# Kernel tuning notes

Measured on AMD Instinct MI355X. Metric: run time of the kernel, lower is better.

The kernel has to match this reference:

```python
import jax, jax.numpy as jnp
import numpy as np

N_NODES = 50000
N_EDGES = 600000
D_IN = 128
H = D_IN // 2  # 64
N_GRAPHS = 500
DIM_TARGET = 1


def setup_inputs() -> dict:
    key = jax.random.key(0)
    ks = jax.random.split(key, 16)
    x = jax.random.normal(ks[0], (N_NODES, D_IN), dtype=jnp.float32)
    edge_index = jax.random.randint(ks[1], (2, N_EDGES), 0, N_NODES, dtype=jnp.int64)
    batch = jnp.sort(jax.random.randint(ks[2], (N_NODES,), 0, N_GRAPHS, dtype=jnp.int64))
    # SAGEConv params: lin_l (neighbor aggregate, with bias), lin_r (root, no bias)
    s = 1.0 / np.sqrt(D_IN)
    Wl = jax.random.uniform(ks[3], (D_IN, H), jnp.float32, -s, s)
    bl = jnp.zeros((H,), jnp.float32)
    Wr = jax.random.uniform(ks[4], (D_IN, H), jnp.float32, -s, s)
    # MLP: 64->32->16->8->1
    dims = [H, H // 2, H // 4, H // 8, DIM_TARGET]
    params = {}
    for i in range(4):
        si = 1.0 / np.sqrt(dims[i])
        params[f"W{i}"] = jax.random.uniform(ks[5 + 2 * i], (dims[i], dims[i + 1]), jnp.float32, -si, si)
        params[f"b{i}"] = jax.random.uniform(ks[6 + 2 * i], (dims[i + 1],), jnp.float32, -si, si)
    return dict(x=x, edge_index=edge_index, batch=batch, Wl=Wl, bl=bl, Wr=Wr, **params)


def reference(x, edge_index, batch, Wl, bl, Wr, W0, b0, W1, b1, W2, b2, W3, b3):
    n_nodes = x.shape[0]
    src, dst = edge_index[0], edge_index[1]
    # SAGEConv mean aggregation: mean of source-node features at each target node
    agg = jax.ops.segment_sum(x[src], dst, num_segments=n_nodes)          # [N, D]
    cnt = jax.ops.segment_sum(jnp.ones((src.shape[0],), x.dtype), dst, num_segments=n_nodes)
    mean_nbr = agg / jnp.maximum(cnt, 1.0)[:, None]
    x1 = mean_nbr @ Wl + bl + x @ Wr                                      # [N, H]
    # global_mean_pool by graph id
    gsum = jax.ops.segment_sum(x1, batch, num_segments=N_GRAPHS)          # [G, H]
    gcnt = jax.ops.segment_sum(jnp.ones((n_nodes,), x.dtype), batch, num_segments=N_GRAPHS)
    h = gsum / jnp.maximum(gcnt, 1.0)[:, None]
    # MLP (dropout is identity in eval mode)
    h = jax.nn.relu(h @ W0 + b0)
    h = jax.nn.relu(h @ W1 + b1)
    h = jax.nn.relu(h @ W2 + b2)
    return h @ W3 + b3
```

## Files before the change

kernel.cpp:

```cpp
#include <hip/hip_runtime.h>
#include <hip/hip_bf16.h>

#define N_NODES  50000
#define N_EDGES  600000
#define D_IN     128
#define H        64
#define N_GRAPHS 500
#define MAXDEG   48

#define PROJ_BLOCKS 782
#define M_TILES     3125
#define SCAT_CHUNKS 512
#define SCAT_BLOCKS (SCAT_CHUNKS * 8)
#define EPC         1172
#define NPS         (N_NODES / 8)
#define GST_BLOCKS  2
#define PX_BLOCKS   500
#define PREP_GRID   (PROJ_BLOCKS + SCAT_BLOCKS + GST_BLOCKS + PX_BLOCKS)

#define SPLIT    16
#define GBLK     (N_GRAPHS * SPLIT)

#define OF_DEG   0
#define MEMSET_B 200704
#define OF_PNP   200704
#define OF_PX    2248704
#define OF_GCNT  2504704
#define OF_GST   2506752
#define OF_COL   2508800
#define OF_YB    7308800

typedef __attribute__((ext_vector_type(8))) short short8;
typedef __attribute__((ext_vector_type(4))) float float4v;

__device__ __forceinline__ float bflo(unsigned int u) { return __uint_as_float(u << 16); }
__device__ __forceinline__ float bfhi(unsigned int u) { return __uint_as_float(u & 0xffff0000u); }
__device__ __forceinline__ unsigned short f2bf(float f) {
    return __bfloat16_as_ushort(__float2bfloat16(f));
}

__global__ __launch_bounds__(256) void prep_kernel(
        const float* __restrict__ x, const float* __restrict__ Wl,
        unsigned short* __restrict__ yb,
        const int* __restrict__ src, const int* __restrict__ dst,
        int* __restrict__ deg, unsigned short* __restrict__ col,
        const int* __restrict__ batch, int* __restrict__ gstart,
        float* __restrict__ Px, int* __restrict__ gcnt) {
    __shared__ float red[512];
    int bid = blockIdx.x, t = threadIdx.x;
    int wave = t >> 6, lane = t & 63;

    if (bid < PROJ_BLOCKS) {
        int mt = bid * 4 + wave;
        if (mt < M_TILES) {
            int c = lane & 15, q = lane >> 4;
            short8 Bf[4][4];
            #pragma unroll
            for (int t4 = 0; t4 < 4; ++t4)
                #pragma unroll
                for (int s4 = 0; s4 < 4; ++s4) {
                    short8 b;
                    #pragma unroll
                    for (int jj = 0; jj < 8; ++jj)
                        b[jj] = (short)f2bf(Wl[(s4 * 32 + q * 8 + jj) * H + t4 * 16 + c]);
                    Bf[t4][s4] = b;
                }
            float4v acc[4] = {};
            const float* xrow = x + ((size_t)mt * 16 + c) * D_IN + q * 8;
            #pragma unroll
            for (int s4 = 0; s4 < 4; ++s4) {
                const float4* ap = (const float4*)(xrow + s4 * 32);
                float4 a0 = ap[0], a1 = ap[1];
                short8 Af;
                Af[0] = (short)f2bf(a0.x); Af[1] = (short)f2bf(a0.y);
                Af[2] = (short)f2bf(a0.z); Af[3] = (short)f2bf(a0.w);
                Af[4] = (short)f2bf(a1.x); Af[5] = (short)f2bf(a1.y);
                Af[6] = (short)f2bf(a1.z); Af[7] = (short)f2bf(a1.w);
                #pragma unroll
                for (int t4 = 0; t4 < 4; ++t4)
                    acc[t4] = __builtin_amdgcn_mfma_f32_16x16x32_bf16(Af, Bf[t4][s4], acc[t4], 0, 0, 0);
            }
            #pragma unroll
            for (int t4 = 0; t4 < 4; ++t4)
                #pragma unroll
                for (int r = 0; r < 4; ++r) {
                    int node = mt * 16 + q * 4 + r;
                    yb[(size_t)node * H + t4 * 16 + c] = f2bf(acc[t4][r]);
                }
        }
    } else if (bid < PROJ_BLOCKS + SCAT_BLOCKS) {
        int shard = bid & 7;
        int chunk = (bid - PROJ_BLOCKS) >> 3;
        int lo = shard * NPS, hi = lo + NPS;
        int e0 = chunk * EPC;
        int e1 = e0 + EPC; if (e1 > N_EDGES) e1 = N_EDGES;
        for (int e = e0 + t; e < e1; e += 256) {
            int d = dst[e];
            if (d >= lo && d < hi) {
                int pos = atomicAdd(&deg[d], 1);
                if (pos < MAXDEG)
                    col[(size_t)d * MAXDEG + pos] = (unsigned short)src[e];
            }
        }
    } else if (bid < PROJ_BLOCKS + SCAT_BLOCKS + GST_BLOCKS) {
        int g = (bid - PROJ_BLOCKS - SCAT_BLOCKS) * 256 + t;
        if (g <= N_GRAPHS) {
            int lo = 0, hi = N_NODES;
            while (lo < hi) {
                int m = (lo + hi) >> 1;
                if (batch[m] < g) lo = m + 1; else hi = m;
            }
            gstart[g] = lo;
        }
    } else {
        int p = bid - PROJ_BLOCKS - SCAT_BLOCKS - GST_BLOCKS;
        int lo = 0, hi = N_NODES;
        while (lo < hi) { int m = (lo + hi) >> 1; if (batch[m] < p) lo = m + 1; else hi = m; }
        int a = lo;
        hi = N_NODES;
        while (lo < hi) { int m = (lo + hi) >> 1; if (batch[m] < p + 1) lo = m + 1; else hi = m; }
        int b = lo;
        float fx = 0.f, fy = 0.f;
        for (int n = a + wave; n < b; n += 4) {
            float2 u = ((const float2*)(x + (size_t)n * D_IN))[lane];
            fx += u.x; fy += u.y;
        }
        red[wave * D_IN + 2 * lane]     = fx;
        red[wave * D_IN + 2 * lane + 1] = fy;
        __syncthreads();
        if (t < D_IN) {
            float v = red[t] + red[D_IN + t] + red[2 * D_IN + t] + red[3 * D_IN + t];
            Px[(size_t)p * D_IN + t] = v;
        }
        if (t == 0) gcnt[p] = b - a;
    }
}

__global__ __launch_bounds__(256) void gather_kernel(
        const unsigned short* __restrict__ yb, const unsigned short* __restrict__ col,
        const int* __restrict__ deg, const int* __restrict__ gstart,
        float* __restrict__ PnP) {
    __shared__ float red[4 * H];
    int bid  = blockIdx.x;
    int wave = threadIdx.x >> 6;
    int lane = threadIdx.x & 63;
    int half = lane >> 5, fp = lane & 31;
    int g = bid >> 4, s = bid & 15;
    int n0 = gstart[g], n1 = gstart[g + 1];
    const unsigned short* yl = yb + 2 * fp;

    float2 pn = make_float2(0.f, 0.f);
    for (int n = n0 + s * 4 + wave; n < n1; n += 4 * SPLIT) {
        int d = deg[n];
        int dl = (d < MAXDEG) ? d : MAXDEG;
        int cidx = (lane < dl) ? (int)col[(size_t)n * MAXDEG + lane] : 0;

        float tx = 0.f, ty = 0.f;
        int j = 0;
        for (; j + 8 <= dl; j += 8) {
            int s0 = __shfl(cidx, j + half),     s1 = __shfl(cidx, j + 2 + half);
            int s2 = __shfl(cidx, j + 4 + half), s3 = __shfl(cidx, j + 6 + half);
            unsigned int u0 = *(const unsigned int*)(yl + (size_t)s0 * H);
            unsigned int u1 = *(const unsigned int*)(yl + (size_t)s1 * H);
            unsigned int u2 = *(const unsigned int*)(yl + (size_t)s2 * H);
            unsigned int u3 = *(const unsigned int*)(yl + (size_t)s3 * H);
            tx += bflo(u0) + bflo(u1) + bflo(u2) + bflo(u3);
            ty += bfhi(u0) + bfhi(u1) + bfhi(u2) + bfhi(u3);
        }
        for (; j + 2 <= dl; j += 2) {
            int s0 = __shfl(cidx, j + half);
            unsigned int u = *(const unsigned int*)(yl + (size_t)s0 * H);
            tx += bflo(u); ty += bfhi(u);
        }
        if (j < dl) {
            int s0 = __shfl(cidx, j);
            if (half == 0) {
                unsigned int u = *(const unsigned int*)(yl + (size_t)s0 * H);
                tx += bflo(u); ty += bfhi(u);
            }
        }
        if (d > 0) {
            float w = __builtin_amdgcn_rcpf((float)d);
            pn.x = fmaf(tx, w, pn.x);
            pn.y = fmaf(ty, w, pn.y);
        }
    }
    pn.x += __shfl_xor(pn.x, 32);
    pn.y += __shfl_xor(pn.y, 32);
    if (half == 0) {
        red[wave * H + 2 * fp]     = pn.x;
        red[wave * H + 2 * fp + 1] = pn.y;
    }
    __syncthreads();
    if (threadIdx.x < H) {
        float v = red[threadIdx.x] + red[H + threadIdx.x]
                + red[2 * H + threadIdx.x] + red[3 * H + threadIdx.x];
        PnP[(size_t)bid * H + threadIdx.x] = v;
    }
}

__global__ void final_kernel(
        const float* __restrict__ PnP, const float* __restrict__ Px,
        const int* __restrict__ gcnt,
        const float* __restrict__ bl, const float* __restrict__ Wr,
        const float* __restrict__ W0, const float* __restrict__ b0,
        const float* __restrict__ W1, const float* __restrict__ b1,
        const float* __restrict__ W2, const float* __restrict__ b2,
        const float* __restrict__ W3, const float* __restrict__ b3,
        float* __restrict__ out) {
    int g = blockIdx.x;
    int t = threadIdx.x;
    __shared__ float sx[D_IN], hs[H], a0[32], a1[16], a2[8];
    sx[t]      = Px[(size_t)g * D_IN + t];
    sx[t + 64] = Px[(size_t)g * D_IN + 64 + t];
    float sp = 0.f;
    {
        const float* base = PnP + ((size_t)g << 4) * H + t;
        #pragma unroll
        for (int s = 0; s < SPLIT; ++s) sp += base[s * H];
    }
    __syncthreads();

    int ng = gcnt[g];
    float acc = sp;
    #pragma unroll 8
    for (int d = 0; d < D_IN; ++d)
        acc += sx[d] * Wr[d * H + t];
    hs[t] = (ng > 0) ? (acc / (float)ng + bl[t]) : 0.f;
    __syncthreads();
    if (t < 32) { float a = b0[t]; for (int d = 0; d < H;  ++d) a += hs[d] * W0[d * 32 + t]; a0[t] = fmaxf(a, 0.f); }
    __syncthreads();
    if (t < 16) { float a = b1[t]; for (int d = 0; d < 32; ++d) a += a0[d] * W1[d * 16 + t]; a1[t] = fmaxf(a, 0.f); }
    __syncthreads();
    if (t < 8)  { float a = b2[t]; for (int d = 0; d < 16; ++d) a += a1[d] * W2[d * 8 + t];  a2[t] = fmaxf(a, 0.f); }
    __syncthreads();
    if (t == 0) { float a = b3[0]; for (int d = 0; d < 8;  ++d) a += a2[d] * W3[d]; out[g] = a; }
}

extern "C" void kernel_launch(void* const* d_in, const int* in_sizes, int n_in,
                              void* d_out, int out_size, void* d_ws, size_t ws_size,
                              hipStream_t stream) {
    const float* x     = (const float*)d_in[0];
    const int*   ei    = (const int*)  d_in[1];
    const int*   batch = (const int*)  d_in[2];
    const float* Wl    = (const float*)d_in[3];
    const float* bl    = (const float*)d_in[4];
    const float* Wr    = (const float*)d_in[5];
    const float* W0    = (const float*)d_in[6];
    const float* b0    = (const float*)d_in[7];
    const float* W1    = (const float*)d_in[8];
    const float* b1    = (const float*)d_in[9];
    const float* W2    = (const float*)d_in[10];
    const float* b2    = (const float*)d_in[11];
    const float* W3    = (const float*)d_in[12];
    const float* b3    = (const float*)d_in[13];
    float* out = (float*)d_out;

    char* ws = (char*)d_ws;
    int*            deg    = (int*)(ws + OF_DEG);
    float*          PnP    = (float*)(ws + OF_PNP);
    float*          Px     = (float*)(ws + OF_PX);
    int*            gcnt   = (int*)(ws + OF_GCNT);
    int*            gstart = (int*)(ws + OF_GST);
    unsigned short* col    = (unsigned short*)(ws + OF_COL);
    unsigned short* yb     = (unsigned short*)(ws + OF_YB);

    hipMemsetAsync(ws, 0, MEMSET_B, stream);

    prep_kernel<<<PREP_GRID, 256, 0, stream>>>(
        x, Wl, yb, ei, ei + N_EDGES, deg, col, batch, gstart, Px, gcnt);
    gather_kernel<<<GBLK, 256, 0, stream>>>(yb, col, deg, gstart, PnP);
    final_kernel<<<N_GRAPHS, 64, 0, stream>>>(PnP, Px, gcnt, bl, Wr,
                                              W0, b0, W1, b1, W2, b2, W3, b3, out);
}
```

Baseline: 171.5 us.

## Fuse root projection into MFMA prep and pool it in gather

The root term x@Wr is now computed per node alongside x@Wl inside the MFMA projection tiles and stored as bf16. The gather kernel sums it per graph next to the neighbour mean, where each wave's half-lanes both add it so it is scaled by 0.5. This removes the separate per-graph x pooling blocks and the 128x64 matvec in the final kernel. The cost is extra MFMA work and weight loads (Wr fragments are now loaded inside the loop rather than hoisted), an extra bf16 write and read of N×64, and bf16 rounding of the root term.

```diff
diff --git a/kernel.cpp b/kernel.cpp
--- a/kernel.cpp
+++ b/kernel.cpp
@@ -15,8 +15,7 @@
 #define EPC         1172
 #define NPS         (N_NODES / 8)
 #define GST_BLOCKS  2
-#define PX_BLOCKS   500
-#define PREP_GRID   (PROJ_BLOCKS + SCAT_BLOCKS + GST_BLOCKS + PX_BLOCKS)
+#define PREP_GRID   (PROJ_BLOCKS + SCAT_BLOCKS + GST_BLOCKS)
 
 #define SPLIT    16
 #define GBLK     (N_GRAPHS * SPLIT)
@@ -24,11 +23,10 @@
 #define OF_DEG   0
 #define MEMSET_B 200704
 #define OF_PNP   200704
-#define OF_PX    2248704
-#define OF_GCNT  2504704
-#define OF_GST   2506752
-#define OF_COL   2508800
-#define OF_YB    7308800
+#define OF_GST   4296704
+#define OF_COL   4298752
+#define OF_YB    9098752
+#define OF_ZB    15498752
 
 typedef __attribute__((ext_vector_type(8))) short short8;
 typedef __attribute__((ext_vector_type(4))) float float4v;
@@ -41,12 +39,11 @@
 
 __global__ __launch_bounds__(256) void prep_kernel(
         const float* __restrict__ x, const float* __restrict__ Wl,
-        unsigned short* __restrict__ yb,
+        const float* __restrict__ Wr,
+        unsigned short* __restrict__ yb, unsigned short* __restrict__ zb,
         const int* __restrict__ src, const int* __restrict__ dst,
         int* __restrict__ deg, unsigned short* __restrict__ col,
-        const int* __restrict__ batch, int* __restrict__ gstart,
-        float* __restrict__ Px, int* __restrict__ gcnt) {
-    __shared__ float red[512];
+        const int* __restrict__ batch, int* __restrict__ gstart) {
     int bid = blockIdx.x, t = threadIdx.x;
     int wave = t >> 6, lane = t & 63;
 
@@ -54,18 +51,8 @@
         int mt = bid * 4 + wave;
         if (mt < M_TILES) {
             int c = lane & 15, q = lane >> 4;
-            short8 Bf[4][4];
-            #pragma unroll
-            for (int t4 = 0; t4 < 4; ++t4)
-                #pragma unroll
-                for (int s4 = 0; s4 < 4; ++s4) {
-                    short8 b;
-                    #pragma unroll
-                    for (int jj = 0; jj < 8; ++jj)
-                        b[jj] = (short)f2bf(Wl[(s4 * 32 + q * 8 + jj) * H + t4 * 16 + c]);
-                    Bf[t4][s4] = b;
-                }
-            float4v acc[4] = {};
+            float4v accY[4] = {};
+            float4v accZ[4] = {};
             const float* xrow = x + ((size_t)mt * 16 + c) * D_IN + q * 8;
             #pragma unroll
             for (int s4 = 0; s4 < 4; ++s4) {
@@ -76,16 +63,28 @@
                 Af[2] = (short)f2bf(a0.z); Af[3] = (short)f2bf(a0.w);
                 Af[4] = (short)f2bf(a1.x); Af[5] = (short)f2bf(a1.y);
                 Af[6] = (short)f2bf(a1.z); Af[7] = (short)f2bf(a1.w);
+                int kb = s4 * 32 + q * 8;
                 #pragma unroll
-                for (int t4 = 0; t4 < 4; ++t4)
-                    acc[t4] = __builtin_amdgcn_mfma_f32_16x16x32_bf16(Af, Bf[t4][s4], acc[t4], 0, 0, 0);
+                for (int t4 = 0; t4 < 4; ++t4) {
+                    const float* wl = Wl + (size_t)kb * H + t4 * 16 + c;
+                    const float* wr = Wr + (size_t)kb * H + t4 * 16 + c;
+                    short8 BL, BR;
+                    #pragma unroll
+                    for (int jj = 0; jj < 8; ++jj) {
+                        BL[jj] = (short)f2bf(wl[jj * H]);
+                        BR[jj] = (short)f2bf(wr[jj * H]);
+                    }
+                    accY[t4] = __builtin_amdgcn_mfma_f32_16x16x32_bf16(Af, BL, accY[t4], 0, 0, 0);
+                    accZ[t4] = __builtin_amdgcn_mfma_f32_16x16x32_bf16(Af, BR, accZ[t4], 0, 0, 0);
+                }
             }
             #pragma unroll
             for (int t4 = 0; t4 < 4; ++t4)
                 #pragma unroll
                 for (int r = 0; r < 4; ++r) {
                     int node = mt * 16 + q * 4 + r;
-                    yb[(size_t)node * H + t4 * 16 + c] = f2bf(acc[t4][r]);
+                    yb[(size_t)node * H + t4 * 16 + c] = f2bf(accY[t4][r]);
+                    zb[(size_t)node * H + t4 * 16 + c] = f2bf(accZ[t4][r]);
                 }
         }
     } else if (bid < PROJ_BLOCKS + SCAT_BLOCKS) {
@@ -102,7 +101,7 @@
                     col[(size_t)d * MAXDEG + pos] = (unsigned short)src[e];
             }
         }
-    } else if (bid < PROJ_BLOCKS + SCAT_BLOCKS + GST_BLOCKS) {
+    } else {
         int g = (bid - PROJ_BLOCKS - SCAT_BLOCKS) * 256 + t;
         if (g <= N_GRAPHS) {
             int lo = 0, hi = N_NODES;
@@ -112,35 +111,15 @@
             }
             gstart[g] = lo;
         }
-    } else {
-        int p = bid - PROJ_BLOCKS - SCAT_BLOCKS - GST_BLOCKS;
-        int lo = 0, hi = N_NODES;
-        while (lo < hi) { int m = (lo + hi) >> 1; if (batch[m] < p) lo = m + 1; else hi = m; }
-        int a = lo;
-        hi = N_NODES;
-        while (lo < hi) { int m = (lo + hi) >> 1; if (batch[m] < p + 1) lo = m + 1; else hi = m; }
-        int b = lo;
-        float fx = 0.f, fy = 0.f;
-        for (int n = a + wave; n < b; n += 4) {
-            float2 u = ((const float2*)(x + (size_t)n * D_IN))[lane];
-            fx += u.x; fy += u.y;
-        }
-        red[wave * D_IN + 2 * lane]     = fx;
-        red[wave * D_IN + 2 * lane + 1] = fy;
-        __syncthreads();
-        if (t < D_IN) {
-            float v = red[t] + red[D_IN + t] + red[2 * D_IN + t] + red[3 * D_IN + t];
-            Px[(size_t)p * D_IN + t] = v;
-        }
-        if (t == 0) gcnt[p] = b - a;
     }
 }
 
 __global__ __launch_bounds__(256) void gather_kernel(
-        const unsigned short* __restrict__ yb, const unsigned short* __restrict__ col,
+        const unsigned short* __restrict__ yb, const unsigned short* __restrict__ zb,
+        const unsigned short* __restrict__ col,
         const int* __restrict__ deg, const int* __restrict__ gstart,
         float* __restrict__ PnP) {
-    __shared__ float red[4 * H];
+    __shared__ float red[8 * H];
     int bid  = blockIdx.x;
     int wave = threadIdx.x >> 6;
     int lane = threadIdx.x & 63;
@@ -150,7 +129,11 @@
     const unsigned short* yl = yb + 2 * fp;
 
     float2 pn = make_float2(0.f, 0.f);
+    float2 pz = make_float2(0.f, 0.f);
     for (int n = n0 + s * 4 + wave; n < n1; n += 4 * SPLIT) {
+        unsigned int uz = *(const unsigned int*)(zb + (size_t)n * H + 2 * fp);
+        pz.x += bflo(uz); pz.y += bfhi(uz);
+
         int d = deg[n];
         int dl = (d < MAXDEG) ? d : MAXDEG;
         int cidx = (lane < dl) ? (int)col[(size_t)n * MAXDEG + lane] : 0;
@@ -187,22 +170,29 @@
     }
     pn.x += __shfl_xor(pn.x, 32);
     pn.y += __shfl_xor(pn.y, 32);
+    pz.x += __shfl_xor(pz.x, 32);
+    pz.y += __shfl_xor(pz.y, 32);
     if (half == 0) {
-        red[wave * H + 2 * fp]     = pn.x;
-        red[wave * H + 2 * fp + 1] = pn.y;
+        red[wave * H + 2 * fp]             = pn.x;
+        red[wave * H + 2 * fp + 1]         = pn.y;
+        red[4 * H + wave * H + 2 * fp]     = pz.x * 0.5f;
+        red[4 * H + wave * H + 2 * fp + 1] = pz.y * 0.5f;
     }
     __syncthreads();
     if (threadIdx.x < H) {
-        float v = red[threadIdx.x] + red[H + threadIdx.x]
-                + red[2 * H + threadIdx.x] + red[3 * H + threadIdx.x];
-        PnP[(size_t)bid * H + threadIdx.x] = v;
+        int i = threadIdx.x;
+        float v = red[i] + red[H + i] + red[2 * H + i] + red[3 * H + i];
+        PnP[(size_t)bid * 2 * H + i] = v;
+    } else if (threadIdx.x < 2 * H) {
+        int i = threadIdx.x - H;
+        float v = red[4 * H + i] + red[5 * H + i] + red[6 * H + i] + red[7 * H + i];
+        PnP[(size_t)bid * 2 * H + H + i] = v;
     }
 }
 
 __global__ void final_kernel(
-        const float* __restrict__ PnP, const float* __restrict__ Px,
-        const int* __restrict__ gcnt,
-        const float* __restrict__ bl, const float* __restrict__ Wr,
+        const float* __restrict__ PnP, const int* __restrict__ gstart,
+        const float* __restrict__ bl,
         const float* __restrict__ W0, const float* __restrict__ b0,
         const float* __restrict__ W1, const float* __restrict__ b1,
         const float* __restrict__ W2, const float* __restrict__ b2,
@@ -210,23 +200,18 @@
         float* __restrict__ out) {
     int g = blockIdx.x;
     int t = threadIdx.x;
-    __shared__ float sx[D_IN], hs[H], a0[32], a1[16], a2[8];
-    sx[t]      = Px[(size_t)g * D_IN + t];
-    sx[t + 64] = Px[(size_t)g * D_IN + 64 + t];
-    float sp = 0.f;
+    __shared__ float hs[H], a0[32], a1[16], a2[8];
+    float sy = 0.f, sz = 0.f;
     {
-        const float* base = PnP + ((size_t)g << 4) * H + t;
+        const float* base = PnP + ((size_t)g << 4) * 2 * H;
         #pragma unroll
-        for (int s = 0; s < SPLIT; ++s) sp += base[s * H];
-    }
-    __syncthreads();
-
-    int ng = gcnt[g];
-    float acc = sp;
-    #pragma unroll 8
-    for (int d = 0; d < D_IN; ++d)
-        acc += sx[d] * Wr[d * H + t];
-    hs[t] = (ng > 0) ? (acc / (float)ng + bl[t]) : 0.f;
+        for (int s = 0; s < SPLIT; ++s) {
+            sy += base[s * 2 * H + t];
+            sz += base[s * 2 * H + H + t];
+        }
+    }
+    int ng = gstart[g + 1] - gstart[g];
+    hs[t] = (ng > 0) ? ((sy + sz) / (float)ng + bl[t]) : 0.f;
     __syncthreads();
     if (t < 32) { float a = b0[t]; for (int d = 0; d < H;  ++d) a += hs[d] * W0[d * 32 + t]; a0[t] = fmaxf(a, 0.f); }
     __syncthreads();
@@ -259,17 +244,16 @@
     char* ws = (char*)d_ws;
     int*            deg    = (int*)(ws + OF_DEG);
     float*          PnP    = (float*)(ws + OF_PNP);
-    float*          Px     = (float*)(ws + OF_PX);
-    int*            gcnt   = (int*)(ws + OF_GCNT);
     int*            gstart = (int*)(ws + OF_GST);
     unsigned short* col    = (unsigned short*)(ws + OF_COL);
     unsigned short* yb     = (unsigned short*)(ws + OF_YB);
+    unsigned short* zb     = (unsigned short*)(ws + OF_ZB);
 
     hipMemsetAsync(ws, 0, MEMSET_B, stream);
 
     prep_kernel<<<PREP_GRID, 256, 0, stream>>>(
-        x, Wl, yb, ei, ei + N_EDGES, deg, col, batch, gstart, Px, gcnt);
-    gather_kernel<<<GBLK, 256, 0, stream>>>(yb, col, deg, gstart, PnP);
-    final_kernel<<<N_GRAPHS, 64, 0, stream>>>(PnP, Px, gcnt, bl, Wr,
+        x, Wl, Wr, yb, zb, ei, ei + N_EDGES, deg, col, batch, gstart);
+    gather_kernel<<<GBLK, 256, 0, stream>>>(yb, zb, col, deg, gstart, PnP);
+    final_kernel<<<N_GRAPHS, 64, 0, stream>>>(PnP, gstart, bl,
                                               W0, b0, W1, b1, W2, b2, W3, b3, out);
 }
```

New measurement: 163.0 us. 1.05x faster.
